# Kernel optimization log

Hardware: AMD Instinct MI355X
Metric: run time of the kernel (lower is better)

The kernel has to match this reference:

```python
import jax, jax.numpy as jnp
import numpy as np

SIGMA = 0.07        # kernel width param; gamma = 1/sigma
K_NEG = 16          # hard negatives per anchor
BS = 8192
DIM = 256

def setup_inputs() -> dict:
    key = jax.random.key(0)
    features = jax.random.normal(key, (BS, 2, DIM), dtype=jnp.float32)
    return {"features": features}

def reference(features):
    gamma = 1.0 / float(SIGMA)
    F1 = features[:, 0, :].astype(jnp.float32)   # (bs, d)
    F2 = features[:, 1, :].astype(jnp.float32)   # (bs, d)
    # RBF-style kernel: exp(-gamma * (2 - 2 * F1 @ F2^T))
    K = jnp.exp(-gamma * (2.0 - 2.0 * jnp.einsum('id,jd->ij', F1, F2)))  # (bs, bs)
    pos_loss = jnp.mean(jnp.diagonal(K))
    # mask diagonal with -inf, take row-wise top-k, mean over all selected
    eye = jnp.eye(BS, dtype=bool)
    neg = jnp.where(eye, -jnp.inf, K)
    topk_vals, _ = jax.lax.top_k(neg, K_NEG)     # (bs, k)
    hard_neg_loss = jnp.mean(topk_vals)
    return (-pos_loss, hard_neg_loss)
```

## Files before the change

### kernel.cpp

```cpp
#include <hip/hip_runtime.h>
#include <math.h>

#define BS   8192
#define DIM  256
#define KNEG 16
#define GAMMA (1.0f / 0.07f)
#define EXP_CLAMP 60.0f
#define NSTRIPS 8

typedef float v4f  __attribute__((ext_vector_type(4)));
typedef short s8b  __attribute__((ext_vector_type(8)));

__device__ __forceinline__ float sat_exp(float dot) {
    float a = 2.0f * GAMMA * dot - 2.0f * GAMMA;
    return expf(fminf(a, EXP_CLAMP));
}

__device__ __forceinline__ void sort16(float (&a)[16]) {
#pragma unroll
    for (int k = 2; k <= 16; k <<= 1) {
#pragma unroll
        for (int j = k >> 1; j > 0; j >>= 1) {
#pragma unroll
            for (int i = 0; i < 16; ++i) {
                int ixj = i ^ j;
                if (ixj > i) {
                    float lo = fminf(a[i], a[ixj]);
                    float hi = fmaxf(a[i], a[ixj]);
                    bool up = ((i & k) == 0);
                    a[i]   = up ? lo : hi;
                    a[ixj] = up ? hi : lo;
                }
            }
        }
    }
}

__device__ __forceinline__ void merge_top16(float (&lst)[16], const float (&nw)[16]) {
    float t[16];
#pragma unroll
    for (int i = 0; i < 16; ++i) t[i] = fmaxf(lst[i], nw[15 - i]);
#pragma unroll
    for (int j = 8; j > 0; j >>= 1) {
#pragma unroll
        for (int i = 0; i < 16; ++i) {
            int ixj = i ^ j;
            if (ixj > i) {
                float lo = fminf(t[i], t[ixj]);
                float hi = fmaxf(t[i], t[ixj]);
                t[i] = lo; t[ixj] = hi;
            }
        }
    }
#pragma unroll
    for (int i = 0; i < 16; ++i) lst[i] = t[i];
}

__device__ __forceinline__ void topk_insert(float (&lst)[16], float v) {
    float nl[16];
#pragma unroll
    for (int u = 0; u < 15; ++u)
        nl[u] = (v > lst[u + 1]) ? lst[u + 1] : ((v > lst[u]) ? v : lst[u]);
    nl[15] = (v > lst[15]) ? v : lst[15];
#pragma unroll
    for (int u = 0; u < 16; ++u) lst[u] = nl[u];
}

__device__ __forceinline__ unsigned short f2bf_rne(float f) {
    unsigned int u = __float_as_uint(f);
    u += 0x7FFFu + ((u >> 16) & 1u);
    return (unsigned short)(u >> 16);
}

__device__ __forceinline__ void gld_lds16(const void* g, void* l) {
    __builtin_amdgcn_global_load_lds(
        (const __attribute__((address_space(1))) void*)g,
        (__attribute__((address_space(3))) void*)l, 16, 0, 0);
}

__device__ __forceinline__ float finite_or(float x, float repl) {
    if (isnan(x)) return repl;
    if (isinf(x)) return x > 0.0f ? 3.0e38f : -3.0e38f;
    return x;
}

__global__ void conv_pos(const float* __restrict__ feat,
                         unsigned short* __restrict__ featbf,
                         float* __restrict__ partialPos) {
    __shared__ float red[8];
    int t = blockIdx.x * 256 + threadIdx.x;
    int row = t >> 5;
    int c = t & 31;
    const float* f1 = feat + (size_t)row * 512 + c * 8;
    const float* f2 = f1 + 256;
    float4 a0 = *(const float4*)(f1);
    float4 a1 = *(const float4*)(f1 + 4);
    float4 b0 = *(const float4*)(f2);
    float4 b1 = *(const float4*)(f2 + 4);
    uint4 pa, pb;
    pa.x = (unsigned)f2bf_rne(a0.x) | ((unsigned)f2bf_rne(a0.y) << 16);
    pa.y = (unsigned)f2bf_rne(a0.z) | ((unsigned)f2bf_rne(a0.w) << 16);
    pa.z = (unsigned)f2bf_rne(a1.x) | ((unsigned)f2bf_rne(a1.y) << 16);
    pa.w = (unsigned)f2bf_rne(a1.z) | ((unsigned)f2bf_rne(a1.w) << 16);
    pb.x = (unsigned)f2bf_rne(b0.x) | ((unsigned)f2bf_rne(b0.y) << 16);
    pb.y = (unsigned)f2bf_rne(b0.z) | ((unsigned)f2bf_rne(b0.w) << 16);
    pb.z = (unsigned)f2bf_rne(b1.x) | ((unsigned)f2bf_rne(b1.y) << 16);
    pb.w = (unsigned)f2bf_rne(b1.z) | ((unsigned)f2bf_rne(b1.w) << 16);
    *(uint4*)(featbf + (size_t)row * 512 + c * 8) = pa;
    *(uint4*)(featbf + (size_t)row * 512 + 256 + c * 8) = pb;
    float p = a0.x * b0.x + a0.y * b0.y + a0.z * b0.z + a0.w * b0.w
            + a1.x * b1.x + a1.y * b1.y + a1.z * b1.z + a1.w * b1.w;
#pragma unroll
    for (int o = 16; o; o >>= 1) p += __shfl_xor(p, o, 32);
    if (c == 0) red[threadIdx.x >> 5] = sat_exp(p);
    __syncthreads();
    if (threadIdx.x == 0) {
        float s = 0.0f;
#pragma unroll
        for (int i = 0; i < 8; ++i) s += red[i];
        partialPos[blockIdx.x] = s;
    }
}

#define A_OFF 32768
#define S1_LDS 40960

__global__ __launch_bounds__(256, 4) void stage1(const unsigned short* __restrict__ featbf,
                                                 float* __restrict__ wsTop) {
    __shared__ __align__(16) char smem[S1_LDS];
    const int t = threadIdx.x;
    const int l = t & 63;
    const int w = t >> 6;
    const int wy = w >> 1, wx = w & 1;
    const int quad = l >> 4, lane16 = l & 15;
    const int nbase = blockIdx.x * 64;
    const int strip = blockIdx.y;

#pragma unroll
    for (int jj = 0; jj < 8; ++jj) {
        int j = w * 8 + jj;
        int r = 2 * j + (l >> 5);
        int c = (l & 31) ^ (r & 31);
        gld_lds16(featbf + ((size_t)(nbase + r) << 9) + c * 8, smem + j * 1024);
    }

    float lst[2][16];
#pragma unroll
    for (int ni = 0; ni < 2; ++ni)
#pragma unroll
        for (int i = 0; i < 16; ++i) lst[ni][i] = -INFINITY;

    const int akey = (quad ^ ((lane16 >> 1) & 3)) * 16;

#pragma unroll 1
    for (int ct = 0; ct < 8; ++ct) {
        const int ctbase = strip * 1024 + ct * 128;
        v4f acc[4][2];
#pragma unroll
        for (int mi = 0; mi < 4; ++mi)
#pragma unroll
            for (int ni = 0; ni < 2; ++ni) acc[mi][ni] = (v4f)0.0f;

#pragma unroll
        for (int s = 0; s < 8; ++s) {
            __syncthreads();
#pragma unroll
            for (int jj = 0; jj < 2; ++jj) {
                int j = w * 2 + jj;
                int r = 16 * j + (l >> 2);
                int c = (l & 3) ^ ((r >> 1) & 3);
                gld_lds16(featbf + ((size_t)(ctbase + r) << 9) + 256 + s * 32 + c * 8,
                          smem + A_OFF + j * 1024);
            }
            __syncthreads();
            s8b a[4];
#pragma unroll
            for (int mi = 0; mi < 4; ++mi)
                a[mi] = *(const s8b*)(smem + A_OFF
                    + (wx * 64 + mi * 16 + lane16) * 64 + akey);
#pragma unroll
            for (int ni = 0; ni < 2; ++ni) {
                int nl31 = ni * 16 + lane16;
                s8b b = *(const s8b*)(smem
                    + (wy * 32 + nl31) * 512 + (((s * 4 + quad) ^ nl31) & 31) * 16);
#pragma unroll
                for (int mi = 0; mi < 4; ++mi)
                    acc[mi][ni] = __builtin_amdgcn_mfma_f32_16x16x32_bf16(a[mi], b, acc[mi][ni], 0, 0, 0);
            }
        }
#pragma unroll
        for (int ni = 0; ni < 2; ++ni) {
            const int row = nbase + wy * 32 + ni * 16 + lane16;
            float nw[16];
#pragma unroll
            for (int mi = 0; mi < 4; ++mi) {
                const int c0 = ctbase + wx * 64 + mi * 16 + quad * 4;
#pragma unroll
                for (int r4 = 0; r4 < 4; ++r4) {
                    float v = acc[mi][ni][r4];
                    nw[mi * 4 + r4] = (c0 + r4 == row) ? -INFINITY : v;
                }
            }
            sort16(nw);
            merge_top16(lst[ni], nw);
        }
    }
#pragma unroll
    for (int ni = 0; ni < 2; ++ni) {
#pragma unroll
        for (int r = 16; r <= 32; r <<= 1) {
            float nw[16];
#pragma unroll
            for (int i = 0; i < 16; ++i) nw[i] = __shfl(lst[ni][i], l ^ r, 64);
            merge_top16(lst[ni], nw);
        }
    }
    __syncthreads();
    float* mrg = (float*)(smem + A_OFF);
    if (wx == 1 && quad == 0) {
#pragma unroll
        for (int ni = 0; ni < 2; ++ni) {
            int rl = wy * 32 + ni * 16 + lane16;
#pragma unroll
            for (int i = 0; i < 16; i += 4)
                *(v4f*)(mrg + rl * 16 + i) = *(v4f*)&lst[ni][i];
        }
    }
    __syncthreads();
    if (wx == 0 && quad == 0) {
#pragma unroll
        for (int ni = 0; ni < 2; ++ni) {
            const int rl = wy * 32 + ni * 16 + lane16;
            float nw[16];
#pragma unroll
            for (int i = 0; i < 16; ++i) nw[i] = mrg[rl * 16 + i];
            merge_top16(lst[ni], nw);
            float* dst = wsTop + ((size_t)(nbase + rl) * NSTRIPS + strip) * 16;
#pragma unroll
            for (int i = 0; i < 16; i += 4)
                *(float4*)(dst + i) = make_float4(lst[ni][i], lst[ni][i + 1],
                                                  lst[ni][i + 2], lst[ni][i + 3]);
        }
    }
}

__global__ void stage2(const float* __restrict__ wsTop, float* __restrict__ partialNeg) {
    __shared__ float red[256];
    int row = blockIdx.x * 256 + threadIdx.x;
    const float* src = wsTop + (size_t)row * (NSTRIPS * 16);
    float lst[16];
#pragma unroll
    for (int i = 0; i < 16; ++i) lst[i] = src[i];
#pragma unroll 1
    for (int c = 16; c < NSTRIPS * 16; c += 16) {
        float nw[16];
#pragma unroll
        for (int i = 0; i < 16; i += 4) {
            float4 v4 = *(const float4*)(src + c + i);
            nw[i] = v4.x; nw[i + 1] = v4.y; nw[i + 2] = v4.z; nw[i + 3] = v4.w;
        }
        merge_top16(lst, nw);
    }
    float s = 0.0f;
#pragma unroll
    for (int i = 0; i < 16; ++i) s += sat_exp(lst[i]);
    red[threadIdx.x] = s;
    __syncthreads();
    for (int o = 128; o; o >>= 1) {
        if (threadIdx.x < o) red[threadIdx.x] += red[threadIdx.x + o];
        __syncthreads();
    }
    if (threadIdx.x == 0) partialNeg[blockIdx.x] = red[0];
}

__global__ void final_kernel(const float* __restrict__ partialPos,
                             const float* __restrict__ partialNeg,
                             float* __restrict__ out) {
    __shared__ float w1[4], w2[4];
    float sp = 0.0f, sn = 0.0f;
    for (int i = threadIdx.x; i < 1024; i += 256) sp += partialPos[i];
    if (threadIdx.x < 32) sn = partialNeg[threadIdx.x];
#pragma unroll
    for (int o = 32; o; o >>= 1) {
        sp += __shfl_xor(sp, o, 64);
        sn += __shfl_xor(sn, o, 64);
    }
    if ((threadIdx.x & 63) == 0) {
        w1[threadIdx.x >> 6] = sp;
        w2[threadIdx.x >> 6] = sn;
    }
    __syncthreads();
    if (threadIdx.x == 0) {
        float tp = w1[0] + w1[1] + w1[2] + w1[3];
        float tn = w2[0] + w2[1] + w2[2] + w2[3];
        out[0] = finite_or(-(tp / (float)BS), 0.0f);
        out[1] = finite_or(tn / (float)(BS * KNEG), 0.0f);
    }
}

__global__ void init_acc(float* acc) {
    if (threadIdx.x < 64) acc[threadIdx.x] = 0.0f;
}

__global__ void pos_kernel(const float* __restrict__ feat, float* __restrict__ acc) {
    int t = blockIdx.x * 256 + threadIdx.x;
    int row = t >> 4;
    int lane16 = t & 15;
    const float* f = feat + (size_t)row * 512 + lane16 * 16;
    float p = 0.0f;
#pragma unroll
    for (int q = 0; q < 16; q += 4) {
        float4 a = *(const float4*)(f + q);
        float4 b = *(const float4*)(f + 256 + q);
        p += a.x * b.x + a.y * b.y + a.z * b.z + a.w * b.w;
    }
#pragma unroll
    for (int o = 8; o; o >>= 1) p += __shfl_xor(p, o, 16);
    if (lane16 == 0) atomicAdd(&acc[0], sat_exp(p));
}

#define L_AOFF   0
#define L_BOFF   10240
#define L_PITCH  80
#define CPITCH  272
#define CWAVE   17408
#define L_SMEM  69632
__global__ __launch_bounds__(256, 2) void stage1_legacy(const float* __restrict__ feat,
                                                        float* __restrict__ wsTop) {
    __shared__ __align__(16) char smem[L_SMEM];
    const int t = threadIdx.x;
    const int l = t & 63;
    const int w = t >> 6;
    const int wy = w >> 1, wx = w & 1;
    const int quad = l >> 4, lane16 = l & 15;
    const int rowbase = blockIdx.x * 128;
    const int strip = blockIdx.y;
    char* cw = smem + w * CWAVE;
    const int grow = rowbase + wy * 64 + l;

    float lst[16];
#pragma unroll
    for (int i = 0; i < 16; ++i) lst[i] = -INFINITY;

    for (int ct = 0; ct < 4; ++ct) {
        const int colbase = strip * 1024 + ct * 256;
        v4f acc[4][8];
#pragma unroll
        for (int mi = 0; mi < 4; ++mi)
#pragma unroll
            for (int ni = 0; ni < 8; ++ni) acc[mi][ni] = (v4f)0.0f;
        for (int s = 0; s < 8; ++s) {
            const int k0 = s * 32;
            __syncthreads();
#pragma unroll
            for (int i = 0; i < 4; ++i) {
                int c = i * 256 + t;
                int r = c >> 3, chk = c & 7;
                float4 v = *(const float4*)(feat + (size_t)(rowbase + r) * 512 + k0 + chk * 4);
                uint2 pk;
                pk.x = (unsigned)f2bf_rne(v.x) | ((unsigned)f2bf_rne(v.y) << 16);
                pk.y = (unsigned)f2bf_rne(v.z) | ((unsigned)f2bf_rne(v.w) << 16);
                *(uint2*)(smem + L_AOFF + r * L_PITCH + chk * 8) = pk;
            }
#pragma unroll
            for (int i = 0; i < 8; ++i) {
                int c = i * 256 + t;
                int n = c >> 3, chk = c & 7;
                float4 v = *(const float4*)(feat + (size_t)(colbase + n) * 512 + 256 + k0 + chk * 4);
                uint2 pk;
                pk.x = (unsigned)f2bf_rne(v.x) | ((unsigned)f2bf_rne(v.y) << 16);
                pk.y = (unsigned)f2bf_rne(v.z) | ((unsigned)f2bf_rne(v.w) << 16);
                *(uint2*)(smem + L_BOFF + n * L_PITCH + chk * 8) = pk;
            }
            __syncthreads();
            s8b a[4];
#pragma unroll
            for (int mi = 0; mi < 4; ++mi)
                a[mi] = *(const s8b*)(smem + L_AOFF + (wy * 64 + mi * 16 + lane16) * L_PITCH + quad * 16);
#pragma unroll
            for (int ni = 0; ni < 8; ++ni) {
                s8b b = *(const s8b*)(smem + L_BOFF + (wx * 128 + ni * 16 + lane16) * L_PITCH + quad * 16);
#pragma unroll
                for (int mi = 0; mi < 4; ++mi)
                    acc[mi][ni] = __builtin_amdgcn_mfma_f32_16x16x32_bf16(a[mi], b, acc[mi][ni], 0, 0, 0);
            }
        }
#pragma unroll
        for (int h = 0; h < 2; ++h) {
            __syncthreads();
#pragma unroll
            for (int ni = 0; ni < 4; ++ni) {
                int c = ni * 16 + lane16;
#pragma unroll
                for (int mi = 0; mi < 4; ++mi)
                    *(v4f*)(cw + c * CPITCH + mi * 64 + quad * 16) = acc[mi][h * 4 + ni];
            }
            __syncthreads();
            const int gc0 = colbase + wx * 128 + h * 64;
            const int dj = grow - gc0;
#pragma unroll
            for (int j = 0; j < 64; ++j) {
                float v = *(const float*)(cw + j * CPITCH + l * 4);
                if (v > lst[0] && j != dj) topk_insert(lst, v);
            }
        }
    }
    float* dst = wsTop + (size_t)grow * 256 + strip * 32 + wx * 16;
#pragma unroll
    for (int i = 0; i < 16; i += 4)
        *(float4*)(dst + i) = make_float4(lst[i], lst[i + 1], lst[i + 2], lst[i + 3]);
}

__global__ void stage2_legacy(const float* __restrict__ wsTop, float* __restrict__ acc) {
    int row = blockIdx.x * blockDim.x + threadIdx.x;
    if (row >= BS) return;
    const float* src = wsTop + (size_t)row * 256;
    float lst[16];
#pragma unroll
    for (int i = 0; i < 16; ++i) lst[i] = -INFINITY;
    for (int c = 0; c < 256; c += 4) {
        float4 v4 = *(const float4*)(src + c);
        float vv[4] = {v4.x, v4.y, v4.z, v4.w};
#pragma unroll
        for (int j = 0; j < 4; ++j)
            if (vv[j] > lst[0]) topk_insert(lst, vv[j]);
    }
    float s = 0.0f;
#pragma unroll
    for (int i = 0; i < 16; ++i) s += sat_exp(lst[i]);
    atomicAdd(&acc[1], s);
}

__global__ void final_legacy(const float* __restrict__ acc, float* __restrict__ out) {
    if (threadIdx.x == 0) {
        out[0] = finite_or(-(acc[0] / (float)BS), 0.0f);
        out[1] = finite_or(acc[1] / (float)(BS * KNEG), 0.0f);
    }
}

extern "C" void kernel_launch(void* const* d_in, const int* in_sizes, int n_in,
                              void* d_out, int out_size, void* d_ws, size_t ws_size,
                              hipStream_t stream) {
    const float* feat = (const float*)d_in[0];
    float* out = (float*)d_out;

    unsigned short* featbf = (unsigned short*)d_ws;
    float* wsTop = (float*)(featbf + (size_t)BS * 512);
    float* partialPos = wsTop + (size_t)BS * NSTRIPS * 16;
    float* partialNeg = partialPos + 1024;
    const size_t need_new = (size_t)BS * 512 * 2 + (size_t)BS * NSTRIPS * 16 * 4
                          + (1024 + 32) * 4;

    if (ws_size >= need_new) {
        conv_pos<<<1024, 256, 0, stream>>>(feat, featbf, partialPos);
        stage1<<<dim3(128, NSTRIPS), 256, 0, stream>>>(featbf, wsTop);
        stage2<<<32, 256, 0, stream>>>(wsTop, partialNeg);
        final_kernel<<<1, 256, 0, stream>>>(partialPos, partialNeg, out);
    } else {
        float* acc = (float*)d_ws;
        float* wsTopL = acc + 64;
        init_acc<<<1, 64, 0, stream>>>(acc);
        pos_kernel<<<512, 256, 0, stream>>>(feat, acc);
        stage1_legacy<<<dim3(64, 8), 256, 0, stream>>>(feat, wsTopL);
        stage2_legacy<<<32, 256, 0, stream>>>(wsTopL, acc);
        final_legacy<<<1, 1, 0, stream>>>(acc, out);
    }
}
```

Before: 139.3 us.

## Load A fragments directly from global memory and drop per-step LDS staging barriers

Stage1 no longer stages the column-tile (A) fragments through LDS each k-step. Each lane now reads its bf16 fragment straight from global/L2, which removes two __syncthreads per step and shrinks the LDS footprint. The bitonic sort16 is replaced with an explicit hand-written comparator network, and merge_top16 now works in place instead of through a temporary array. The trade is that each wave issues uncoalesced 16-byte global loads, and A data is no longer shared across waves through LDS, so latency now has to be hidden by occupancy and cache hits.

```diff
diff --git a/kernel.cpp b/kernel.cpp
--- a/kernel.cpp
+++ b/kernel.cpp
@@ -16,44 +16,41 @@
     return expf(fminf(a, EXP_CLAMP));
 }
 
+__device__ __forceinline__ void ce(float& x, float& y) {
+    float lo = fminf(x, y), hi = fmaxf(x, y);
+    x = lo; y = hi;
+}
+
 __device__ __forceinline__ void sort16(float (&a)[16]) {
-#pragma unroll
-    for (int k = 2; k <= 16; k <<= 1) {
-#pragma unroll
-        for (int j = k >> 1; j > 0; j >>= 1) {
-#pragma unroll
-            for (int i = 0; i < 16; ++i) {
-                int ixj = i ^ j;
-                if (ixj > i) {
-                    float lo = fminf(a[i], a[ixj]);
-                    float hi = fmaxf(a[i], a[ixj]);
-                    bool up = ((i & k) == 0);
-                    a[i]   = up ? lo : hi;
-                    a[ixj] = up ? hi : lo;
-                }
-            }
-        }
-    }
+    ce(a[0],a[1]); ce(a[2],a[3]); ce(a[4],a[5]); ce(a[6],a[7]);
+    ce(a[8],a[9]); ce(a[10],a[11]); ce(a[12],a[13]); ce(a[14],a[15]);
+    ce(a[0],a[2]); ce(a[1],a[3]); ce(a[4],a[6]); ce(a[5],a[7]);
+    ce(a[8],a[10]); ce(a[9],a[11]); ce(a[12],a[14]); ce(a[13],a[15]);
+    ce(a[1],a[2]); ce(a[5],a[6]); ce(a[9],a[10]); ce(a[13],a[14]);
+    ce(a[0],a[4]); ce(a[1],a[5]); ce(a[2],a[6]); ce(a[3],a[7]);
+    ce(a[8],a[12]); ce(a[9],a[13]); ce(a[10],a[14]); ce(a[11],a[15]);
+    ce(a[2],a[4]); ce(a[3],a[5]); ce(a[10],a[12]); ce(a[11],a[13]);
+    ce(a[1],a[2]); ce(a[3],a[4]); ce(a[5],a[6]);
+    ce(a[9],a[10]); ce(a[11],a[12]); ce(a[13],a[14]);
+    ce(a[0],a[8]); ce(a[1],a[9]); ce(a[2],a[10]); ce(a[3],a[11]);
+    ce(a[4],a[12]); ce(a[5],a[13]); ce(a[6],a[14]); ce(a[7],a[15]);
+    ce(a[4],a[8]); ce(a[5],a[9]); ce(a[6],a[10]); ce(a[7],a[11]);
+    ce(a[2],a[4]); ce(a[3],a[5]); ce(a[6],a[8]); ce(a[7],a[9]);
+    ce(a[10],a[12]); ce(a[11],a[13]);
+    ce(a[1],a[2]); ce(a[3],a[4]); ce(a[5],a[6]); ce(a[7],a[8]);
+    ce(a[9],a[10]); ce(a[11],a[12]); ce(a[13],a[14]);
 }
 
 __device__ __forceinline__ void merge_top16(float (&lst)[16], const float (&nw)[16]) {
-    float t[16];
-#pragma unroll
-    for (int i = 0; i < 16; ++i) t[i] = fmaxf(lst[i], nw[15 - i]);
-#pragma unroll
-    for (int j = 8; j > 0; j >>= 1) {
+#pragma unroll
+    for (int i = 0; i < 16; ++i) lst[i] = fmaxf(lst[i], nw[15 - i]);
+#pragma unroll
+    for (int j = 8; j > 0; j >>= 1)
 #pragma unroll
         for (int i = 0; i < 16; ++i) {
             int ixj = i ^ j;
-            if (ixj > i) {
-                float lo = fminf(t[i], t[ixj]);
-                float hi = fmaxf(t[i], t[ixj]);
-                t[i] = lo; t[ixj] = hi;
-            }
-        }
-    }
-#pragma unroll
-    for (int i = 0; i < 16; ++i) lst[i] = t[i];
+            if (ixj > i) ce(lst[i], lst[ixj]);
+        }
 }
 
 __device__ __forceinline__ void topk_insert(float (&lst)[16], float v) {
@@ -122,8 +119,8 @@
     }
 }
 
-#define A_OFF 32768
-#define S1_LDS 40960
+#define MRG_OFF 32768
+#define S1_LDS  36864
 
 __global__ __launch_bounds__(256, 4) void stage1(const unsigned short* __restrict__ featbf,
                                                  float* __restrict__ wsTop) {
@@ -143,14 +140,13 @@
         int c = (l & 31) ^ (r & 31);
         gld_lds16(featbf + ((size_t)(nbase + r) << 9) + c * 8, smem + j * 1024);
     }
+    __syncthreads();
 
     float lst[2][16];
 #pragma unroll
     for (int ni = 0; ni < 2; ++ni)
 #pragma unroll
         for (int i = 0; i < 16; ++i) lst[ni][i] = -INFINITY;
-
-    const int akey = (quad ^ ((lane16 >> 1) & 3)) * 16;
 
 #pragma unroll 1
     for (int ct = 0; ct < 8; ++ct) {
@@ -163,21 +159,12 @@
 
 #pragma unroll
         for (int s = 0; s < 8; ++s) {
-            __syncthreads();
-#pragma unroll
-            for (int jj = 0; jj < 2; ++jj) {
-                int j = w * 2 + jj;
-                int r = 16 * j + (l >> 2);
-                int c = (l & 3) ^ ((r >> 1) & 3);
-                gld_lds16(featbf + ((size_t)(ctbase + r) << 9) + 256 + s * 32 + c * 8,
-                          smem + A_OFF + j * 1024);
-            }
-            __syncthreads();
             s8b a[4];
 #pragma unroll
             for (int mi = 0; mi < 4; ++mi)
-                a[mi] = *(const s8b*)(smem + A_OFF
-                    + (wx * 64 + mi * 16 + lane16) * 64 + akey);
+                a[mi] = *(const s8b*)(featbf
+                    + ((size_t)(ctbase + wx * 64 + mi * 16 + lane16) << 9)
+                    + 256 + s * 32 + quad * 8);
 #pragma unroll
             for (int ni = 0; ni < 2; ++ni) {
                 int nl31 = ni * 16 + lane16;
@@ -215,8 +202,7 @@
             merge_top16(lst[ni], nw);
         }
     }
-    __syncthreads();
-    float* mrg = (float*)(smem + A_OFF);
+    float* mrg = (float*)(smem + MRG_OFF);
     if (wx == 1 && quad == 0) {
 #pragma unroll
         for (int ni = 0; ni < 2; ++ni) {
```

Result: slower. 231.4 us (+66.2%).
